# Performance work log

Measured on AMD Instinct MI355X. Metric: run time of the kernel, lower is better.

Reference implementation:

```python
import jax, jax.numpy as jnp
import numpy as np

EPS = 1e-5

def _conv3x3(x, w, b):
    # standard 3x3 conv, stride 1, padding 1, NCHW/OIHW
    y = jax.lax.conv_general_dilated(x, w, window_strides=(1, 1), padding=((1, 1), (1, 1)),
                                     dimension_numbers=('NCHW', 'OIHW', 'NCHW'))
    return y + b[None, :, None, None]

def _deform_sample(x, offset):
    # x: [B,C,H,W], offset: [B,2*9,H,W] (per kernel point: (dy,dx), torchvision layout)
    # returns bilinear-sampled im2col columns [B,C,9,H,W] with zero padding outside
    B, C, H, W = x.shape
    off = offset.reshape(B, 9, 2, H, W)
    off_y, off_x = off[:, :, 0], off[:, :, 1]                      # [B,9,H,W]
    k = jnp.arange(9)
    ky = (k // 3 - 1).astype(x.dtype)                               # kernel dy in {-1,0,1}
    kx = (k % 3 - 1).astype(x.dtype)                                # kernel dx in {-1,0,1}
    py = jnp.arange(H, dtype=x.dtype)[None, None, :, None] + ky[None, :, None, None] + off_y
    px = jnp.arange(W, dtype=x.dtype)[None, None, None, :] + kx[None, :, None, None] + off_x
    y0 = jnp.floor(py)
    x0 = jnp.floor(px)
    xf = x.reshape(B, C, H * W)
    acc = jnp.zeros((B, C, 9, H, W), x.dtype)
    for dy in (0.0, 1.0):
        for dx in (0.0, 1.0):
            iy = y0 + dy
            ix = x0 + dx
            wgt = (1.0 - jnp.abs(py - iy)) * (1.0 - jnp.abs(px - ix))
            valid = (iy >= 0) & (iy <= H - 1) & (ix >= 0) & (ix <= W - 1)
            wgt = jnp.where(valid, wgt, 0.0)
            idx = jnp.clip(iy, 0, H - 1).astype(jnp.int32) * W + jnp.clip(ix, 0, W - 1).astype(jnp.int32)
            g = jax.vmap(lambda xb, ib: jnp.take(xb, ib, axis=1))(xf, idx.reshape(B, -1))
            acc = acc + wgt[:, None] * g.reshape(B, C, 9, H, W)
    return acc

def setup_inputs() -> dict:
    key = jax.random.key(0)
    ks = jax.random.split(key, 9)
    B, C, O, H, W = 8, 64, 64, 160, 160
    x = jax.random.normal(ks[0], (B, C, H, W), jnp.float32)
    w_off = jax.random.normal(ks[1], (18, C, 3, 3), jnp.float32) * 0.01
    b_off = jax.random.normal(ks[2], (18,), jnp.float32) * 0.01
    w_dcn = jax.random.normal(ks[3], (O, C, 3, 3), jnp.float32) / np.sqrt(C * 9)
    b_dcn = jax.random.normal(ks[4], (O,), jnp.float32) * 0.01
    gamma = 1.0 + 0.1 * jax.random.normal(ks[5], (O,), jnp.float32)
    beta = 0.1 * jax.random.normal(ks[6], (O,), jnp.float32)
    run_mean = 0.1 * jax.random.normal(ks[7], (O,), jnp.float32)
    run_var = 0.5 + jax.random.uniform(ks[8], (O,), jnp.float32)
    return {"x": x, "w_off": w_off, "b_off": b_off, "w_dcn": w_dcn, "b_dcn": b_dcn,
            "gamma": gamma, "beta": beta, "run_mean": run_mean, "run_var": run_var}

def reference(x, w_off, b_off, w_dcn, b_dcn, gamma, beta, run_mean, run_var):
    offset = _conv3x3(x, w_off, b_off)                  # [B,18,H,W]
    cols = _deform_sample(x, offset)                    # [B,C,9,H,W]
    O = w_dcn.shape[0]
    z = jnp.einsum('bckhw,ock->bohw', cols, w_dcn.reshape(O, -1, 9)) + b_dcn[None, :, None, None]
    inv = gamma / jnp.sqrt(run_var + EPS)               # eval-mode BatchNorm
    y = z * inv[None, :, None, None] + (beta - run_mean * inv)[None, :, None, None]
    return jax.nn.relu(y)
```

## Files before the change

### kernel.cpp

```cpp
#include <hip/hip_runtime.h>

#define Hh 160
#define Ww 160
#define HW 25600
#define Bb 8
#define Cc 64
#define Oo 64
#define NPIX (Bb * HW)

#define TROWS 8
#define TCOLS 36
#define TPIX (TROWS * TCOLS)

typedef __bf16 bf16x8 __attribute__((ext_vector_type(8)));
typedef float  f32x4  __attribute__((ext_vector_type(4)));
typedef float  f32x2  __attribute__((ext_vector_type(2)));

__device__ inline unsigned rnd_bf(float a) {
    unsigned u = __float_as_uint(a);
    return (u + 0x7FFFu + ((u >> 16) & 1u)) >> 16;
}
__device__ inline unsigned pack_bf2(float a, float b) {
    unsigned ua = __float_as_uint(a) + 0x8000u;
    unsigned ub = __float_as_uint(b) + 0x8000u;
    return __builtin_amdgcn_perm(ub, ua, 0x07060302);
}
__device__ inline f32x2 up2(unsigned u) {
    f32x2 r;
    r.x = __uint_as_float(u << 16);
    r.y = __uint_as_float(u & 0xffff0000u);
    return r;
}
__device__ inline unsigned blend4(unsigned u00, unsigned u01, unsigned u10, unsigned u11,
                                  float w00, float w01, float w10, float w11) {
    f32x2 r = up2(u00) * w00 + up2(u01) * w01 + up2(u10) * w10 + up2(u11) * w11;
    return pack_bf2(r.x, r.y);
}
union UV { uint4 u; bf16x8 v; };
__device__ inline bf16x8 as_bf(uint4 u) { UV c; c.u = u; return c.v; }

__global__ __launch_bounds__(256) void prep_kernel(
    const float* __restrict__ w_dcn, const float* __restrict__ b_dcn,
    const float* __restrict__ w_off,
    const float* __restrict__ gamma, const float* __restrict__ beta,
    const float* __restrict__ run_mean, const float* __restrict__ run_var,
    unsigned short* __restrict__ wtbf, unsigned short* __restrict__ wofbf,
    float* __restrict__ scaleb)
{
    int i = blockIdx.x * 256 + threadIdx.x;
    if (i < 9 * 8 * 64 * 8) {
        int j = i & 7, l = (i >> 3) & 63, f = (i >> 9) & 7, k = i >> 12;
        int o  = ((f >> 1) << 4) | (l & 15);
        int cc = ((l >> 4) << 3) + ((f & 1) << 5) + j;
        wtbf[i] = (unsigned short)rnd_bf(w_dcn[(o * Cc + cc) * 9 + k]);
    }
    if (i < 9 * 4 * 64 * 8) {
        int j = i & 7, l = (i >> 3) & 63, f = (i >> 9) & 3, k = i >> 11;
        int o  = ((f >> 1) << 4) | (l & 15);
        int cc = ((l >> 4) << 3) + ((f & 1) << 5) + j;
        float v = (o < 18) ? w_off[(o * Cc + cc) * 9 + k] : 0.0f;
        wofbf[i] = (unsigned short)rnd_bf(v);
    }
    if (i < Oo) {
        float inv = gamma[i] * rsqrtf(run_var[i] + 1e-5f);
        scaleb[i]      = inv;
        scaleb[Oo + i] = b_dcn[i] * inv + (beta[i] - run_mean[i] * inv);
    }
}

#define TRD(PIX, LO, HI) do {                                                  \
    int _pp = (PIX);                                                           \
    int _s  = _pp & 7;                                                         \
    const char* _tb = (const char*)tile + _pp * 128;                           \
    LO = *(const uint4*)(_tb + ((quad ^ _s) << 4));                            \
    HI = *(const uint4*)(_tb + (((quad + 4) ^ _s) << 4));                      \
} while (0)

#define GATHF(CY, CX, A, H) do {                                               \
    const float* _sp = xbf + (size_t)(quad * 8) * HW + ((CY) * Ww + (CX));     \
    A = make_uint4(pack_bf2(_sp[0],      _sp[HW]),                             \
                   pack_bf2(_sp[2 * HW], _sp[3 * HW]),                         \
                   pack_bf2(_sp[4 * HW], _sp[5 * HW]),                         \
                   pack_bf2(_sp[6 * HW], _sp[7 * HW]));                        \
    const float* _hp = _sp + (size_t)32 * HW;                                  \
    H = make_uint4(pack_bf2(_hp[0],      _hp[HW]),                             \
                   pack_bf2(_hp[2 * HW], _hp[3 * HW]),                         \
                   pack_bf2(_hp[4 * HW], _hp[5 * HW]),                         \
                   pack_bf2(_hp[6 * HW], _hp[7 * HW]));                        \
} while (0)

__global__ __launch_bounds__(512, 6) void dcn_kernel(
    const float* __restrict__ x,
    const unsigned short* __restrict__ wtbf,
    const unsigned short* __restrict__ wofbf,
    const float* __restrict__ b_off,
    const float* __restrict__ scaleb,
    float* __restrict__ out)
{
    __shared__ __align__(16) unsigned short tile[TPIX * 64];
    __shared__ __align__(16) float offb[128 * 20];

    const int t = threadIdx.x;
    const int lane = t & 63, wv = t >> 6;
    const int m = lane & 15, quad = lane >> 4;

    int blk = blockIdx.x;
    int b   = blk & 7;
    int nb  = blk >> 3;
    int h0  = (nb / 5) * 4;
    int w0  = (nb % 5) * 32;

    const int rloc  = wv >> 1;
    const int chalf = (wv & 1) * 16;
    const int h = h0 + rloc;
    const int w = w0 + chalf + m;
    const int pl_base = rloc * 32 + chalf;

    const float* xbf = x + (size_t)b * Cc * HW;

#pragma unroll
    for (int it = 0; it < 18; ++it) {
        int id  = t + it * 512;
        int col = id % 36;
        int rr  = id / 36;
        int r   = rr & 7;
        int c2  = rr >> 3;
        int yr = min(max(h0 - 2 + r, 0), Hh - 1);
        int xc = min(max(w0 - 2 + col, 0), Ww - 1);
        const float* sp = xbf + (size_t)(c2 * 2) * HW + (yr * Ww + xc);
        unsigned v = pack_bf2(sp[0], sp[HW]);
        int pix = r * TCOLS + col;
        *(unsigned*)((char*)tile + pix * 128
                     + ((((c2 >> 2) ^ (pix & 7)) << 4) + ((c2 & 3) << 2))) = v;
    }
    __syncthreads();

    f32x4 oa0 = {0,0,0,0}, oa1 = {0,0,0,0};
#pragma unroll
    for (int k = 0; k < 9; ++k) {
        int hp = h + k / 3 - 1, wp = w + (k % 3) - 1;
        bool ok = (hp >= 0) & (hp < Hh) & (wp >= 0) & (wp < Ww);
        int r = min(max(hp, 0), Hh - 1) - h0 + 2;
        int c = min(max(wp, 0), Ww - 1) - w0 + 2;
        uint4 r0, r1;
        TRD(r * TCOLS + c, r0, r1);
        if (!ok) { r0 = make_uint4(0,0,0,0); r1 = make_uint4(0,0,0,0); }
        bf16x8 a0 = as_bf(r0), a1 = as_bf(r1);

        const unsigned short* wf = wofbf + (size_t)(k * 4) * 512 + lane * 8;
        bf16x8 b00 = *(const bf16x8*)(wf);
        bf16x8 b01 = *(const bf16x8*)(wf + 512);
        bf16x8 b10 = *(const bf16x8*)(wf + 1024);
        bf16x8 b11 = *(const bf16x8*)(wf + 1536);
        oa0 = __builtin_amdgcn_mfma_f32_16x16x32_bf16(a0, b00, oa0, 0, 0, 0);
        oa0 = __builtin_amdgcn_mfma_f32_16x16x32_bf16(a1, b01, oa0, 0, 0, 0);
        oa1 = __builtin_amdgcn_mfma_f32_16x16x32_bf16(a0, b10, oa1, 0, 0, 0);
        oa1 = __builtin_amdgcn_mfma_f32_16x16x32_bf16(a1, b11, oa1, 0, 0, 0);
    }

    {
        float bo0 = b_off[m];
        float bo1 = (m < 2) ? b_off[16 + m] : 0.0f;
#pragma unroll
        for (int r = 0; r < 4; ++r) {
            int pp = pl_base + quad * 4 + r;
            offb[pp * 20 + m] = oa0[r] + bo0;
            if (m < 2) offb[pp * 20 + 16 + m] = oa1[r] + bo1;
        }
    }
    float oy[9], ox[9];
    {
        const int p20 = (pl_base + m) * 20;
#pragma unroll
        for (int k = 0; k < 9; ++k) {
            f32x2 o = *(const f32x2*)&offb[p20 + 2 * k];
            oy[k] = o.x; ox[k] = o.y;
        }
    }

    f32x4 c0 = {0,0,0,0}, c1 = {0,0,0,0}, c2 = {0,0,0,0}, c3 = {0,0,0,0};
#pragma unroll
    for (int k = 0; k < 9; ++k) {
        float py = (float)(h + k / 3 - 1) + oy[k];
        float px = (float)(w + k % 3 - 1) + ox[k];
        float y0f = floorf(py), x0f = floorf(px);
        float fy = py - y0f, fx = px - x0f;
        int y0 = (int)y0f, x0i = (int)x0f;
        int y1 = y0 + 1, x1 = x0i + 1;
        bool vy0 = (y0 >= 0) & (y0 < Hh), vy1 = (y1 >= 0) & (y1 < Hh);
        bool vx0 = (x0i >= 0) & (x0i < Ww), vx1 = (x1 >= 0) & (x1 < Ww);
        float w00 = (vy0 & vx0) ? (1.0f - fy) * (1.0f - fx) : 0.0f;
        float w01 = (vy0 & vx1) ? (1.0f - fy) * fx : 0.0f;
        float w10 = (vy1 & vx0) ? fy * (1.0f - fx) : 0.0f;
        float w11 = (vy1 & vx1) ? fy * fx : 0.0f;
        int cy0 = min(max(y0, 0), Hh - 1), cy1 = min(max(y1, 0), Hh - 1);
        int cx0 = min(max(x0i, 0), Ww - 1), cx1 = min(max(x1, 0), Ww - 1);

        int r0 = cy0 - h0 + 2, r1 = cy1 - h0 + 2;
        int d0 = cx0 - w0 + 2, d1 = cx1 - w0 + 2;
        int inw = ((unsigned)r0 <= 7u) & ((unsigned)r1 <= 7u) &
                  ((unsigned)d0 <= 35u) & ((unsigned)d1 <= 35u);

        uint4 a00, h00, a01, h01, a10, h10, a11, h11;
        if (__all(inw)) {
            TRD(r0 * TCOLS + d0, a00, h00);
            TRD(r0 * TCOLS + d1, a01, h01);
            TRD(r1 * TCOLS + d0, a10, h10);
            TRD(r1 * TCOLS + d1, a11, h11);
        } else {
            GATHF(cy0, cx0, a00, h00);
            GATHF(cy0, cx1, a01, h01);
            GATHF(cy1, cx0, a10, h10);
            GATHF(cy1, cx1, a11, h11);
        }

        uint4 o0, o1;
        o0.x = blend4(a00.x, a01.x, a10.x, a11.x, w00, w01, w10, w11);
        o0.y = blend4(a00.y, a01.y, a10.y, a11.y, w00, w01, w10, w11);
        o0.z = blend4(a00.z, a01.z, a10.z, a11.z, w00, w01, w10, w11);
        o0.w = blend4(a00.w, a01.w, a10.w, a11.w, w00, w01, w10, w11);
        o1.x = blend4(h00.x, h01.x, h10.x, h11.x, w00, w01, w10, w11);
        o1.y = blend4(h00.y, h01.y, h10.y, h11.y, w00, w01, w10, w11);
        o1.z = blend4(h00.z, h01.z, h10.z, h11.z, w00, w01, w10, w11);
        o1.w = blend4(h00.w, h01.w, h10.w, h11.w, w00, w01, w10, w11);
        bf16x8 A0 = as_bf(o0), A1 = as_bf(o1);

        const unsigned short* wf = wtbf + (size_t)(k * 8) * 512 + lane * 8;
        bf16x8 B0, B1;
        B0 = *(const bf16x8*)(wf);
        B1 = *(const bf16x8*)(wf + 512);
        c0 = __builtin_amdgcn_mfma_f32_16x16x32_bf16(A0, B0, c0, 0, 0, 0);
        c0 = __builtin_amdgcn_mfma_f32_16x16x32_bf16(A1, B1, c0, 0, 0, 0);
        B0 = *(const bf16x8*)(wf + 1024);
        B1 = *(const bf16x8*)(wf + 1536);
        c1 = __builtin_amdgcn_mfma_f32_16x16x32_bf16(A0, B0, c1, 0, 0, 0);
        c1 = __builtin_amdgcn_mfma_f32_16x16x32_bf16(A1, B1, c1, 0, 0, 0);
        B0 = *(const bf16x8*)(wf + 2048);
        B1 = *(const bf16x8*)(wf + 2560);
        c2 = __builtin_amdgcn_mfma_f32_16x16x32_bf16(A0, B0, c2, 0, 0, 0);
        c2 = __builtin_amdgcn_mfma_f32_16x16x32_bf16(A1, B1, c2, 0, 0, 0);
        B0 = *(const bf16x8*)(wf + 3072);
        B1 = *(const bf16x8*)(wf + 3584);
        c3 = __builtin_amdgcn_mfma_f32_16x16x32_bf16(A0, B0, c3, 0, 0, 0);
        c3 = __builtin_amdgcn_mfma_f32_16x16x32_bf16(A1, B1, c3, 0, 0, 0);
    }

    __syncthreads();
    float* obuf = (float*)tile;
#pragma unroll
    for (int nt = 0; nt < 4; ++nt) {
        f32x4 a = (nt == 0) ? c0 : (nt == 1) ? c1 : (nt == 2) ? c2 : c3;
        int o = nt * 16 + m;
        float sc = scaleb[o];
        float bs = scaleb[Oo + o];
        f32x4 r;
        r[0] = fmaxf(a[0] * sc + bs, 0.0f);
        r[1] = fmaxf(a[1] * sc + bs, 0.0f);
        r[2] = fmaxf(a[2] * sc + bs, 0.0f);
        r[3] = fmaxf(a[3] * sc + bs, 0.0f);
        *(f32x4*)&obuf[o * 132 + pl_base + quad * 4] = r;
    }
    __syncthreads();
    {
        int o = t >> 3, part = t & 7;
        const float* src = obuf + o * 132 + part * 16;
        float* dst = out + ((size_t)b * Oo + o) * HW
                   + (h0 + (part >> 1)) * Ww + w0 + (part & 1) * 16;
        float4 v0 = *(const float4*)(src);
        float4 v1 = *(const float4*)(src + 4);
        float4 v2 = *(const float4*)(src + 8);
        float4 v3 = *(const float4*)(src + 12);
        *(float4*)(dst)      = v0;
        *(float4*)(dst + 4)  = v1;
        *(float4*)(dst + 8)  = v2;
        *(float4*)(dst + 12) = v3;
    }
}

extern "C" void kernel_launch(void* const* d_in, const int* in_sizes, int n_in,
                              void* d_out, int out_size, void* d_ws, size_t ws_size,
                              hipStream_t stream) {
    const float* x        = (const float*)d_in[0];
    const float* w_off    = (const float*)d_in[1];
    const float* b_off    = (const float*)d_in[2];
    const float* w_dcn    = (const float*)d_in[3];
    const float* b_dcn    = (const float*)d_in[4];
    const float* gamma    = (const float*)d_in[5];
    const float* beta     = (const float*)d_in[6];
    const float* run_mean = (const float*)d_in[7];
    const float* run_var  = (const float*)d_in[8];
    float* out = (float*)d_out;

    unsigned short* wtbf  = (unsigned short*)d_ws;
    unsigned short* wofbf = wtbf + 9 * 8 * 64 * 8;
    float* scaleb         = (float*)(wofbf + 9 * 4 * 64 * 8);

    prep_kernel<<<(9 * 8 * 64 * 8 + 255) / 256, 256, 0, stream>>>(
        w_dcn, b_dcn, w_off, gamma, beta, run_mean, run_var, wtbf, wofbf, scaleb);

    dcn_kernel<<<NPIX / 128, 512, 0, stream>>>(x, wtbf, wofbf, b_off, scaleb, out);
}
```

Measured before the change: 209.7 us.

## Use hardware bf16 pack, shuffle offsets in registers, raise occupancy, coalesce stores

```diff
diff --git a/kernel.cpp b/kernel.cpp
--- a/kernel.cpp
+++ b/kernel.cpp
@@ -20,10 +20,10 @@
     unsigned u = __float_as_uint(a);
     return (u + 0x7FFFu + ((u >> 16) & 1u)) >> 16;
 }
-__device__ inline unsigned pack_bf2(float a, float b) {
-    unsigned ua = __float_as_uint(a) + 0x8000u;
-    unsigned ub = __float_as_uint(b) + 0x8000u;
-    return __builtin_amdgcn_perm(ub, ua, 0x07060302);
+__device__ inline unsigned cvtpk(float a, float b) {
+    unsigned r;
+    asm("v_cvt_pk_bf16_f32 %0, %1, %2" : "=v"(r) : "v"(a), "v"(b));
+    return r;
 }
 __device__ inline f32x2 up2(unsigned u) {
     f32x2 r;
@@ -34,7 +34,7 @@
 __device__ inline unsigned blend4(unsigned u00, unsigned u01, unsigned u10, unsigned u11,
                                   float w00, float w01, float w10, float w11) {
     f32x2 r = up2(u00) * w00 + up2(u01) * w01 + up2(u10) * w10 + up2(u11) * w11;
-    return pack_bf2(r.x, r.y);
+    return cvtpk(r.x, r.y);
 }
 union UV { uint4 u; bf16x8 v; };
 __device__ inline bf16x8 as_bf(uint4 u) { UV c; c.u = u; return c.v; }
@@ -78,18 +78,18 @@
 
 #define GATHF(CY, CX, A, H) do {                                               \
     const float* _sp = xbf + (size_t)(quad * 8) * HW + ((CY) * Ww + (CX));     \
-    A = make_uint4(pack_bf2(_sp[0],      _sp[HW]),                             \
-                   pack_bf2(_sp[2 * HW], _sp[3 * HW]),                         \
-                   pack_bf2(_sp[4 * HW], _sp[5 * HW]),                         \
-                   pack_bf2(_sp[6 * HW], _sp[7 * HW]));                        \
+    A = make_uint4(cvtpk(_sp[0],      _sp[HW]),                                \
+                   cvtpk(_sp[2 * HW], _sp[3 * HW]),                            \
+                   cvtpk(_sp[4 * HW], _sp[5 * HW]),                            \
+                   cvtpk(_sp[6 * HW], _sp[7 * HW]));                           \
     const float* _hp = _sp + (size_t)32 * HW;                                  \
-    H = make_uint4(pack_bf2(_hp[0],      _hp[HW]),                             \
-                   pack_bf2(_hp[2 * HW], _hp[3 * HW]),                         \
-                   pack_bf2(_hp[4 * HW], _hp[5 * HW]),                         \
-                   pack_bf2(_hp[6 * HW], _hp[7 * HW]));                        \
+    H = make_uint4(cvtpk(_hp[0],      _hp[HW]),                                \
+                   cvtpk(_hp[2 * HW], _hp[3 * HW]),                            \
+                   cvtpk(_hp[4 * HW], _hp[5 * HW]),                            \
+                   cvtpk(_hp[6 * HW], _hp[7 * HW]));                           \
 } while (0)
 
-__global__ __launch_bounds__(512, 6) void dcn_kernel(
+__global__ __launch_bounds__(512, 8) void dcn_kernel(
     const float* __restrict__ x,
     const unsigned short* __restrict__ wtbf,
     const unsigned short* __restrict__ wofbf,
@@ -98,7 +98,6 @@
     float* __restrict__ out)
 {
     __shared__ __align__(16) unsigned short tile[TPIX * 64];
-    __shared__ __align__(16) float offb[128 * 20];
 
     const int t = threadIdx.x;
     const int lane = t & 63, wv = t >> 6;
@@ -128,7 +127,7 @@
         int yr = min(max(h0 - 2 + r, 0), Hh - 1);
         int xc = min(max(w0 - 2 + col, 0), Ww - 1);
         const float* sp = xbf + (size_t)(c2 * 2) * HW + (yr * Ww + xc);
-        unsigned v = pack_bf2(sp[0], sp[HW]);
+        unsigned v = cvtpk(sp[0], sp[HW]);
         int pix = r * TCOLS + col;
         *(unsigned*)((char*)tile + pix * 128
                      + ((((c2 >> 2) ^ (pix & 7)) << 4) + ((c2 & 3) << 2))) = v;
@@ -152,30 +151,22 @@
         bf16x8 b01 = *(const bf16x8*)(wf + 512);
         bf16x8 b10 = *(const bf16x8*)(wf + 1024);
         bf16x8 b11 = *(const bf16x8*)(wf + 1536);
-        oa0 = __builtin_amdgcn_mfma_f32_16x16x32_bf16(a0, b00, oa0, 0, 0, 0);
-        oa0 = __builtin_amdgcn_mfma_f32_16x16x32_bf16(a1, b01, oa0, 0, 0, 0);
-        oa1 = __builtin_amdgcn_mfma_f32_16x16x32_bf16(a0, b10, oa1, 0, 0, 0);
-        oa1 = __builtin_amdgcn_mfma_f32_16x16x32_bf16(a1, b11, oa1, 0, 0, 0);
-    }
-
-    {
-        float bo0 = b_off[m];
-        float bo1 = (m < 2) ? b_off[16 + m] : 0.0f;
-#pragma unroll
-        for (int r = 0; r < 4; ++r) {
-            int pp = pl_base + quad * 4 + r;
-            offb[pp * 20 + m] = oa0[r] + bo0;
-            if (m < 2) offb[pp * 20 + 16 + m] = oa1[r] + bo1;
-        }
-    }
+        oa0 = __builtin_amdgcn_mfma_f32_16x16x32_bf16(b00, a0, oa0, 0, 0, 0);
+        oa0 = __builtin_amdgcn_mfma_f32_16x16x32_bf16(b01, a1, oa0, 0, 0, 0);
+        oa1 = __builtin_amdgcn_mfma_f32_16x16x32_bf16(b10, a0, oa1, 0, 0, 0);
+        oa1 = __builtin_amdgcn_mfma_f32_16x16x32_bf16(b11, a1, oa1, 0, 0, 0);
+    }
+
     float oy[9], ox[9];
-    {
-        const int p20 = (pl_base + m) * 20;
-#pragma unroll
-        for (int k = 0; k < 9; ++k) {
-            f32x2 o = *(const f32x2*)&offb[p20 + 2 * k];
-            oy[k] = o.x; ox[k] = o.y;
-        }
+#pragma unroll
+    for (int k = 0; k < 9; ++k) {
+        int cy = 2 * k, cx = 2 * k + 1;
+        float vy = (cy < 16) ? __shfl(oa0[cy & 3], ((cy >> 2) << 4) + m, 64)
+                             : __shfl(oa1[(cy - 16) & 3], (((cy - 16) >> 2) << 4) + m, 64);
+        float vx = (cx < 16) ? __shfl(oa0[cx & 3], ((cx >> 2) << 4) + m, 64)
+                             : __shfl(oa1[(cx - 16) & 3], (((cx - 16) >> 2) << 4) + m, 64);
+        oy[k] = vy + b_off[cy];
+        ox[k] = vx + b_off[cx];
     }
 
     f32x4 c0 = {0,0,0,0}, c1 = {0,0,0,0}, c2 = {0,0,0,0}, c3 = {0,0,0,0};
@@ -262,18 +253,14 @@
     }
     __syncthreads();
     {
-        int o = t >> 3, part = t & 7;
-        const float* src = obuf + o * 132 + part * 16;
-        float* dst = out + ((size_t)b * Oo + o) * HW
-                   + (h0 + (part >> 1)) * Ww + w0 + (part & 1) * 16;
-        float4 v0 = *(const float4*)(src);
-        float4 v1 = *(const float4*)(src + 4);
-        float4 v2 = *(const float4*)(src + 8);
-        float4 v3 = *(const float4*)(src + 12);
-        *(float4*)(dst)      = v0;
-        *(float4*)(dst + 4)  = v1;
-        *(float4*)(dst + 8)  = v2;
-        *(float4*)(dst + 12) = v3;
+        int o = t >> 3, c8 = t & 7;
+        const float* src = obuf + o * 132 + c8 * 4;
+        float* dst = out + ((size_t)b * Oo + o) * HW + h0 * Ww + w0 + c8 * 4;
+#pragma unroll
+        for (int j = 0; j < 4; ++j) {
+            float4 v = *(const float4*)(src + j * 32);
+            *(float4*)(dst + (size_t)j * Ww) = v;
+        }
     }
 }
 
```

New measurement: 289.9 us. 38.2% more time.
